# Kernel optimization log

Measured on AMD Instinct MI355X. Metric: run time of the kernel, lower is better.

Reference implementation:

```python
import jax, jax.numpy as jnp
import numpy as np

N = 131072

def _project(feat, x, y):
    # bilinear sample: feat is [H, W, C], x/y are float pixel coords [N]
    x1 = jnp.floor(x); x2 = jnp.ceil(x)
    y1 = jnp.floor(y); y2 = jnp.ceil(y)
    xi1 = x1.astype(jnp.int32); xi2 = x2.astype(jnp.int32)
    yi1 = y1.astype(jnp.int32); yi2 = y2.astype(jnp.int32)
    # JAX clamps out-of-range gather indices (matches GPU tf.gather_nd edge behavior)
    Q11 = feat[xi1, yi1]
    Q12 = feat[xi1, yi2]
    Q21 = feat[xi2, yi1]
    Q22 = feat[xi2, yi2]
    w11 = ((x2 - x) * (y2 - y))[:, None]
    w21 = ((x - x1) * (y2 - y))[:, None]
    w12 = ((x2 - x) * (y - y1))[:, None]
    w22 = ((x - x1) * (y - y1))[:, None]
    return w11 * Q11 + w21 * Q21 + w12 * Q12 + w22 * Q22


def setup_inputs() -> dict:
    key = jax.random.key(0)
    k1, k2, k3, k4, k5 = jax.random.split(key, 5)
    coord = jax.random.normal(k1, (N, 3), dtype=jnp.float32)
    # ensure points are in front of the camera (Z < 0) as assumed by the projection
    coord = coord.at[:, 2].set(-jnp.abs(coord[:, 2]) - 1.0)
    feat1 = jax.random.normal(k2, (56, 56, 64), dtype=jnp.float32)
    feat2 = jax.random.normal(k3, (28, 28, 128), dtype=jnp.float32)
    feat3 = jax.random.normal(k4, (14, 14, 256), dtype=jnp.float32)
    feat4 = jax.random.normal(k5, (7, 7, 512), dtype=jnp.float32)
    return {"coord": coord, "feat1": feat1, "feat2": feat2, "feat3": feat3, "feat4": feat4}


def reference(coord, feat1, feat2, feat3, feat4):
    X = coord[:, 0]; Y = coord[:, 1]; Z = coord[:, 2]
    h = 248.0 * (-Y / -Z) + 112.0
    w = 248.0 * (X / -Z) + 112.0
    h = jnp.clip(h, 0.0, 223.0)
    w = jnp.clip(w, 0.0, 223.0)
    out1 = _project(feat1, h / (224.0 / 56), w / (224.0 / 56))
    out2 = _project(feat2, h / (224.0 / 28), w / (224.0 / 28))
    out3 = _project(feat3, h / (224.0 / 14), w / (224.0 / 14))
    out4 = _project(feat4, h / (224.0 / 7), w / (224.0 / 7))
    return jnp.concatenate([coord, out1, out2, out3, out4], axis=1)
```

## Files before the change

### kernel.cpp

```cpp
#include <hip/hip_runtime.h>


template <int C, int G>
__device__ __forceinline__ void project_level(const float* __restrict__ f,
                                              float x, float y,
                                              float* __restrict__ o, int lane) {
    float x1 = floorf(x), x2 = ceilf(x);
    float y1 = floorf(y), y2 = ceilf(y);
    int xi1 = (int)x1, xi2 = (int)x2;
    int yi1 = (int)y1, yi2 = (int)y2;
    xi1 = min(xi1, G - 1); xi2 = min(xi2, G - 1);
    yi1 = min(yi1, G - 1); yi2 = min(yi2, G - 1);

    float wx2 = x2 - x, wx1 = x - x1;
    float wy2 = y2 - y, wy1 = y - y1;
    float w11 = wx2 * wy2;
    float w21 = wx1 * wy2;
    float w12 = wx2 * wy1;
    float w22 = wx1 * wy1;

    const float* q11 = f + (size_t)(xi1 * G + yi1) * C;
    const float* q12 = f + (size_t)(xi1 * G + yi2) * C;
    const float* q21 = f + (size_t)(xi2 * G + yi1) * C;
    const float* q22 = f + (size_t)(xi2 * G + yi2) * C;

#pragma unroll
    for (int c = lane; c < C; c += 64) {
        float v = w11 * q11[c] + w21 * q21[c] + w12 * q12[c] + w22 * q22[c];
        o[c] = v;
    }
}

__global__ void __launch_bounds__(256)
graph_projection_kernel(const float* __restrict__ coord,
                        const float* __restrict__ f1,
                        const float* __restrict__ f2,
                        const float* __restrict__ f3,
                        const float* __restrict__ f4,
                        float* __restrict__ out, int n) {
    const int lane = threadIdx.x & 63;
    const int wid  = (blockIdx.x * blockDim.x + threadIdx.x) >> 6;
    const int nw   = (gridDim.x * blockDim.x) >> 6;

    for (int p = wid; p < n; p += nw) {
        float X = coord[3 * p + 0];
        float Y = coord[3 * p + 1];
        float Z = coord[3 * p + 2];
        float h = 248.0f * (Y / Z) + 112.0f;
        float w = 248.0f * (X / (-Z)) + 112.0f;
        h = fminf(fmaxf(h, 0.0f), 223.0f);
        w = fminf(fmaxf(w, 0.0f), 223.0f);

        float* orow = out + (size_t)p * 963;
        if (lane < 3) orow[lane] = coord[3 * p + lane];

        project_level<64, 56>(f1, h * 0.25f,    w * 0.25f,    orow + 3,   lane);
        project_level<128, 28>(f2, h * 0.125f,  w * 0.125f,   orow + 67,  lane);
        project_level<256, 14>(f3, h * 0.0625f, w * 0.0625f,  orow + 195, lane);
        project_level<512, 7>(f4, h * 0.03125f, w * 0.03125f, orow + 451, lane);
    }
}

extern "C" void kernel_launch(void* const* d_in, const int* in_sizes, int n_in,
                              void* d_out, int out_size, void* d_ws, size_t ws_size,
                              hipStream_t stream) {
    const float* coord = (const float*)d_in[0];
    const float* f1 = (const float*)d_in[1];
    const float* f2 = (const float*)d_in[2];
    const float* f3 = (const float*)d_in[3];
    const float* f4 = (const float*)d_in[4];
    float* out = (float*)d_out;

    const int n = in_sizes[0] / 3;

    dim3 block(256);
    dim3 grid(2048);
    graph_projection_kernel<<<grid, block, 0, stream>>>(coord, f1, f2, f3, f4, out, n);
}
```

Before: 619.7 us.

## Vectorize bilinear gathers to float4 and process four points per wavefront

Feature maps are now read as float4 vectors, and each wavefront handles a group of four points. Lanes are split across points for the narrow levels (16 lanes per point at 64 channels, 32 lanes at 128) so all 64 lanes do work. Outputs are written with nontemporal stores, using only 4-byte alignment because each row is 963 floats wide. The goal is fewer memory instructions, full lane use on small levels and less cache pollution from the large output stream. The cost is misaligned vector stores and a scalar tail loop.

```diff
diff --git a/kernel.cpp b/kernel.cpp
--- a/kernel.cpp
+++ b/kernel.cpp
@@ -1,63 +1,145 @@
 #include <hip/hip_runtime.h>
 
 
+typedef float f4 __attribute__((ext_vector_type(4)));
+typedef f4 uf4 __attribute__((aligned(4)));
+
+struct BL {
+    f4  wt;
+    int b11, b21, b12, b22;
+};
+
 template <int C, int G>
-__device__ __forceinline__ void project_level(const float* __restrict__ f,
-                                              float x, float y,
-                                              float* __restrict__ o, int lane) {
+__device__ __forceinline__ BL make_bl(float x, float y) {
     float x1 = floorf(x), x2 = ceilf(x);
     float y1 = floorf(y), y2 = ceilf(y);
-    int xi1 = (int)x1, xi2 = (int)x2;
-    int yi1 = (int)y1, yi2 = (int)y2;
-    xi1 = min(xi1, G - 1); xi2 = min(xi2, G - 1);
-    yi1 = min(yi1, G - 1); yi2 = min(yi2, G - 1);
-
+    int xi1 = min((int)x1, G - 1), xi2 = min((int)x2, G - 1);
+    int yi1 = min((int)y1, G - 1), yi2 = min((int)y2, G - 1);
     float wx2 = x2 - x, wx1 = x - x1;
     float wy2 = y2 - y, wy1 = y - y1;
-    float w11 = wx2 * wy2;
-    float w21 = wx1 * wy2;
-    float w12 = wx2 * wy1;
-    float w22 = wx1 * wy1;
+    BL r;
+    r.wt = (f4){wx2 * wy2, wx1 * wy2, wx2 * wy1, wx1 * wy1};
+    const int W = C / 4;
+    r.b11 = (xi1 * G + yi1) * W;
+    r.b21 = (xi2 * G + yi1) * W;
+    r.b12 = (xi1 * G + yi2) * W;
+    r.b22 = (xi2 * G + yi2) * W;
+    return r;
+}
 
-    const float* q11 = f + (size_t)(xi1 * G + yi1) * C;
-    const float* q12 = f + (size_t)(xi1 * G + yi2) * C;
-    const float* q21 = f + (size_t)(xi2 * G + yi1) * C;
-    const float* q22 = f + (size_t)(xi2 * G + yi2) * C;
+__device__ __forceinline__ f4 blend(const f4* __restrict__ f, const BL& b, int cc) {
+    f4 q11 = f[b.b11 + cc];
+    f4 q21 = f[b.b21 + cc];
+    f4 q12 = f[b.b12 + cc];
+    f4 q22 = f[b.b22 + cc];
+    return b.wt.x * q11 + b.wt.y * q21 + b.wt.z * q12 + b.wt.w * q22;
+}
 
-#pragma unroll
-    for (int c = lane; c < C; c += 64) {
-        float v = w11 * q11[c] + w21 * q21[c] + w12 * q12[c] + w22 * q22[c];
-        o[c] = v;
-    }
+__device__ __forceinline__ void proj_hw(const float* __restrict__ coord, int p,
+                                        float& h, float& w) {
+    float X = coord[3 * p + 0];
+    float Y = coord[3 * p + 1];
+    float Z = coord[3 * p + 2];
+    float hh = 248.0f * (Y / Z) + 112.0f;
+    float ww = 248.0f * (X / (-Z)) + 112.0f;
+    h = fminf(fmaxf(hh, 0.0f), 223.0f);
+    w = fminf(fmaxf(ww, 0.0f), 223.0f);
 }
 
 __global__ void __launch_bounds__(256)
-graph_projection_kernel(const float* __restrict__ coord,
-                        const float* __restrict__ f1,
-                        const float* __restrict__ f2,
-                        const float* __restrict__ f3,
-                        const float* __restrict__ f4,
-                        float* __restrict__ out, int n) {
+graph_projection_v2(const float* __restrict__ coord,
+                    const f4* __restrict__ f1, const f4* __restrict__ f2,
+                    const f4* __restrict__ f3, const f4* __restrict__ f4p,
+                    float* __restrict__ out, int n) {
     const int lane = threadIdx.x & 63;
     const int wid  = (blockIdx.x * blockDim.x + threadIdx.x) >> 6;
     const int nw   = (gridDim.x * blockDim.x) >> 6;
+    const int ngrp = n >> 2;
 
-    for (int p = wid; p < n; p += nw) {
-        float X = coord[3 * p + 0];
-        float Y = coord[3 * p + 1];
-        float Z = coord[3 * p + 2];
-        float h = 248.0f * (Y / Z) + 112.0f;
-        float w = 248.0f * (X / (-Z)) + 112.0f;
-        h = fminf(fmaxf(h, 0.0f), 223.0f);
-        w = fminf(fmaxf(w, 0.0f), 223.0f);
+    for (int g = wid; g < ngrp; g += nw) {
+        const int q = g * 4;
+        float h[4], w[4];
+#pragma unroll
+        for (int j = 0; j < 4; ++j) proj_hw(coord, q + j, h[j], w[j]);
 
-        float* orow = out + (size_t)p * 963;
-        if (lane < 3) orow[lane] = coord[3 * p + lane];
+        if (lane < 12) {
+            int j = lane / 3, k = lane - 3 * j;
+            __builtin_nontemporal_store(coord[3 * q + lane],
+                                        out + (size_t)963 * (q + j) + k);
+        }
 
-        project_level<64, 56>(f1, h * 0.25f,    w * 0.25f,    orow + 3,   lane);
-        project_level<128, 28>(f2, h * 0.125f,  w * 0.125f,   orow + 67,  lane);
-        project_level<256, 14>(f3, h * 0.0625f, w * 0.0625f,  orow + 195, lane);
-        project_level<512, 7>(f4, h * 0.03125f, w * 0.03125f, orow + 451, lane);
+        {
+            float hj = (lane & 32) ? ((lane & 16) ? h[3] : h[2])
+                                   : ((lane & 16) ? h[1] : h[0]);
+            float wj = (lane & 32) ? ((lane & 16) ? w[3] : w[2])
+                                   : ((lane & 16) ? w[1] : w[0]);
+            BL b = make_bl<64, 56>(hj * 0.25f, wj * 0.25f);
+            f4 v = blend(f1, b, lane & 15);
+            int j = lane >> 4;
+            __builtin_nontemporal_store(
+                v, (uf4*)(out + (size_t)963 * (q + j) + 3 + 4 * (lane & 15)));
+        }
+
+#pragma unroll
+        for (int jj = 0; jj < 2; ++jj) {
+            float hj = (lane & 32) ? h[2 * jj + 1] : h[2 * jj];
+            float wj = (lane & 32) ? w[2 * jj + 1] : w[2 * jj];
+            BL b = make_bl<128, 28>(hj * 0.125f, wj * 0.125f);
+            f4 v = blend(f2, b, lane & 31);
+            int j = 2 * jj + (lane >> 5);
+            __builtin_nontemporal_store(
+                v, (uf4*)(out + (size_t)963 * (q + j) + 67 + 4 * (lane & 31)));
+        }
+
+#pragma unroll
+        for (int j = 0; j < 4; ++j) {
+            BL b = make_bl<256, 14>(h[j] * 0.0625f, w[j] * 0.0625f);
+            f4 v = blend(f3, b, lane);
+            __builtin_nontemporal_store(
+                v, (uf4*)(out + (size_t)963 * (q + j) + 195 + 4 * lane));
+        }
+
+#pragma unroll
+        for (int j = 0; j < 4; ++j) {
+            BL b = make_bl<512, 7>(h[j] * 0.03125f, w[j] * 0.03125f);
+            f4 v0 = blend(f4p, b, lane);
+            f4 v1 = blend(f4p, b, lane + 64);
+            float* base = out + (size_t)963 * (q + j) + 451;
+            __builtin_nontemporal_store(v0, (uf4*)(base + 4 * lane));
+            __builtin_nontemporal_store(v1, (uf4*)(base + 256 + 4 * lane));
+        }
+    }
+
+    for (int p = (n & ~3) + wid; p < n; p += nw) {
+        float h0, w0;
+        proj_hw(coord, p, h0, w0);
+        if (lane < 3) out[(size_t)963 * p + lane] = coord[3 * p + lane];
+        {
+            BL b = make_bl<64, 56>(h0 * 0.25f, w0 * 0.25f);
+            if (lane < 16) {
+                f4 v = blend(f1, b, lane);
+                *(uf4*)(out + (size_t)963 * p + 3 + 4 * lane) = v;
+            }
+        }
+        {
+            BL b = make_bl<128, 28>(h0 * 0.125f, w0 * 0.125f);
+            if (lane < 32) {
+                f4 v = blend(f2, b, lane);
+                *(uf4*)(out + (size_t)963 * p + 67 + 4 * lane) = v;
+            }
+        }
+        {
+            BL b = make_bl<256, 14>(h0 * 0.0625f, w0 * 0.0625f);
+            f4 v = blend(f3, b, lane);
+            *(uf4*)(out + (size_t)963 * p + 195 + 4 * lane) = v;
+        }
+        {
+            BL b = make_bl<512, 7>(h0 * 0.03125f, w0 * 0.03125f);
+            f4 v0 = blend(f4p, b, lane);
+            f4 v1 = blend(f4p, b, lane + 64);
+            *(uf4*)(out + (size_t)963 * p + 451 + 4 * lane) = v0;
+            *(uf4*)(out + (size_t)963 * p + 451 + 256 + 4 * lane) = v1;
+        }
     }
 }
 
@@ -65,15 +147,15 @@
                               void* d_out, int out_size, void* d_ws, size_t ws_size,
                               hipStream_t stream) {
     const float* coord = (const float*)d_in[0];
-    const float* f1 = (const float*)d_in[1];
-    const float* f2 = (const float*)d_in[2];
-    const float* f3 = (const float*)d_in[3];
-    const float* f4 = (const float*)d_in[4];
+    const f4* f1 = (const f4*)d_in[1];
+    const f4* f2 = (const f4*)d_in[2];
+    const f4* f3 = (const f4*)d_in[3];
+    const f4* f4p = (const f4*)d_in[4];
     float* out = (float*)d_out;
 
     const int n = in_sizes[0] / 3;
 
     dim3 block(256);
     dim3 grid(2048);
-    graph_projection_kernel<<<grid, block, 0, stream>>>(coord, f1, f2, f3, f4, out, n);
+    graph_projection_v2<<<grid, block, 0, stream>>>(coord, f1, f2, f3, f4p, out, n);
 }
```

Result: faster. 582.9 us (-5.9%).
